# Kernel tuning notes

Hardware: AMD Instinct MI355X
Metric: run time of the kernel (lower is better)

## Reference

```python
import jax, jax.numpy as jnp
import numpy as np

HID = 256
NUM_LAYERS = 2


def setup_inputs() -> dict:
    key = jax.random.key(0)
    k0, k1, k2, k3 = jax.random.split(key, 4)
    B, R, C, I = 64, 32, 32, 8
    stdv = 1.0 / np.sqrt(HID)
    inp = jax.random.normal(k0, (B, R, C, I), jnp.float32)
    W_first = jax.random.uniform(k1, (6 * HID, I + 2 * HID), jnp.float32, -stdv, stdv)
    W_other = jax.random.uniform(k2, (NUM_LAYERS - 1, 6 * HID, 4 * HID), jnp.float32, -stdv, stdv)
    Bias = jax.random.uniform(k3, (NUM_LAYERS, 6 * HID), jnp.float32, -stdv, stdv)
    return {"input": inp, "W_first": W_first, "W_other": W_other, "Bias": Bias,
            "batch_size": B, "input_size": I, "flag": 0}


def _run_layer(a, W, b, H):
    # a: [R, B, L, F_in] diagonally-shifted input; W: [6H, F_in+2H]; b: [6H]
    R, Bb, L, _ = a.shape
    C = L - R + 1
    h0 = jnp.zeros((R, Bb, H), a.dtype)

    def step(carry, inputs):
        h_row, h_col = carry
        x_t, t = inputs
        z = jnp.concatenate([h_row, h_col, x_t], axis=-1)        # [R,B,2H+F]
        gate = jnp.einsum('rbf,gf->rbg', z, W)                   # [R,B,6H]
        # torch: bias added only to first B*(t+1) rows, and only when t < R
        mask = ((jnp.arange(R) <= t) & (t < R))[:, None, None]
        gate = jnp.where(mask, gate + b, gate)
        sig = jax.nn.sigmoid(gate[..., :4 * H])
        tnh = jnp.tanh(gate[..., 4 * H:])
        u_r, o_r, u_c, o_c = jnp.split(sig, 4, axis=-1)
        i_r, i_c = jnp.split(tnh, 2, axis=-1)
        h_row = jnp.tanh((1 - u_r) * h_row + u_r * i_r) * o_r
        h_col = jnp.tanh((1 - u_c) * h_col + u_c * i_c) * o_c
        out = jnp.concatenate([h_row, h_col], axis=-1)           # [R,B,2H]
        # row state that would be saved at this step (valid for t >= C-1)
        row_save = jax.lax.dynamic_index_in_dim(
            h_row, jnp.clip(t - (C - 1), 0, R - 1), axis=0, keepdims=False)
        col_save = h_col[R - 1]                                  # saved pre-roll
        h_col = jnp.roll(h_col, 1, axis=0)                       # roll by batch_size == shift slice axis by 1
        return (h_row, h_col), (out, row_save, col_save)

    xs = (jnp.moveaxis(a, 2, 0), jnp.arange(L))
    _, (outs, row_saves, col_saves) = jax.lax.scan(step, (h0, h0), xs)
    a_next = jnp.moveaxis(outs, 0, 2)        # [R, B, L, 2H]
    hidden_row = row_saves[C - 1:]           # [R, B, H]  (steps t >= C-1)
    hidden_col = col_saves[R - 1:]           # [C, B, H]  (steps t >= R-1)
    return a_next, hidden_row, hidden_col


def _forward(input, W_first, W_other, Bias, flag):
    H = Bias.shape[-1] // 6
    num_layers = Bias.shape[0]
    x = jnp.transpose(input, (2, 0, 1, 3)) if flag == 1 else jnp.transpose(input, (1, 0, 2, 3))
    R, Bb, C, I = x.shape
    L = R + C - 1
    # input_transfer[r, :, r:r+C, :] = x[r]  -> pad then roll each slice by r
    xp = jnp.pad(x, ((0, 0), (0, 0), (0, R - 1), (0, 0)))        # [R,B,L,I]
    a = jax.vmap(lambda xr, r: jnp.roll(xr, r, axis=1))(xp, jnp.arange(R))
    rows, cols = [], []
    for layer in range(num_layers):
        W = W_first if layer == 0 else W_other[layer - 1]
        a, hr, hc = _run_layer(a, W, Bias[layer], H)             # dropout=0 / eval: identity
        rows.append(hr)
        cols.append(hc)
    output_all = a.reshape(R * Bb, L, 2 * H)
    hidden_row_all = jnp.transpose(jnp.stack(rows), (2, 0, 1, 3))  # [B, NL, R, H]
    hidden_col_all = jnp.transpose(jnp.stack(cols), (2, 0, 1, 3))  # [B, NL, C, H]
    if flag == 1:
        return output_all, hidden_col_all, hidden_row_all
    return output_all, hidden_row_all, hidden_col_all


def reference(input, W_first, W_other, Bias, batch_size, input_size, flag):
    return _forward(input, W_first, W_other, Bias, flag)
```

## Files before the change

### kernel.cpp

```cpp
#include <hip/hip_runtime.h>

typedef __bf16 bf16x8 __attribute__((ext_vector_type(8)));
typedef float  f32x4  __attribute__((ext_vector_type(4)));

#define Z0S 520
#define Z1S 1032
#define W0P_ELEMS (2 * 8 * 17 * 6 * 512)
#define W1P_ELEMS (2 * 8 * 32 * 6 * 512)
#define XB_ELEMS (2 * 64 * 32 * 512)

__device__ __forceinline__ unsigned short f2bf(float f) {
    unsigned int u = __builtin_bit_cast(unsigned int, f);
    u += 0x7fffu + ((u >> 16) & 1u);
    return (unsigned short)(u >> 16);
}
__device__ __forceinline__ float sigm(float x) {
    x = fminf(30.f, fmaxf(-30.f, x));
    return __fdividef(1.0f, 1.0f + __expf(-x));
}
__device__ __forceinline__ float ftanh(float x) {
    x = fminf(15.f, fmaxf(-15.f, x));
    float e = __expf(2.0f * x);
    return 1.0f - __fdividef(2.0f, e + 1.0f);
}
__device__ __forceinline__ bf16x8 zero8() {
    bf16x8 v;
#pragma unroll
    for (int i = 0; i < 8; ++i) v[i] = (__bf16)0.0f;
    return v;
}
__device__ __forceinline__ void st_f32_wt(float* p, float v) {
    __hip_atomic_store(p, v, __ATOMIC_RELAXED, __HIP_MEMORY_SCOPE_AGENT);
}
__device__ __forceinline__ void st_u16_wt(unsigned short* p, unsigned short v) {
    __hip_atomic_store(p, v, __ATOMIC_RELAXED, __HIP_MEMORY_SCOPE_AGENT);
}

__global__ void convert_w(const float* __restrict__ W0f, const float* __restrict__ W1f,
                          unsigned short* __restrict__ W0p, unsigned short* __restrict__ W1p,
                          int* __restrict__ flags) {
    const int gid = blockIdx.x * blockDim.x + threadIdx.x;
    const int stride = gridDim.x * blockDim.x;
    if (gid < 512) flags[gid] = 0;
    for (int i = gid; i < W0P_ELEMS; i += stride) {
        const int e = i & 7, lane = (i >> 3) & 63;
        const int r = i >> 9;
        const int G = r % 6;  const int r2 = r / 6;
        const int ks = r2 % 17; const int gcg = r2 / 17;
        const int jj = gcg * 16 + (lane & 15);
        const int k = ks * 32 + (lane >> 4) * 8 + e;
        float v = 0.f;
        if (k < 520) v = W0f[(size_t)(G * 256 + jj) * 520 + k];
        W0p[i] = f2bf(v);
    }
    for (int i = gid; i < W1P_ELEMS; i += stride) {
        const int e = i & 7, lane = (i >> 3) & 63;
        const int r = i >> 9;
        const int G = r % 6;  const int r2 = r / 6;
        const int ks = r2 & 31; const int gcg = r2 >> 5;
        const int jj = gcg * 16 + (lane & 15);
        const int k = ks * 32 + (lane >> 4) * 8 + e;
        W1p[i] = f2bf(W1f[(size_t)(G * 256 + jj) * 1024 + k]);
    }
}

__global__ __launch_bounds__(512, 2) void witran_coop(
    const float* __restrict__ inp,
    const unsigned short* __restrict__ W0p,
    const unsigned short* __restrict__ W1p,
    const float* __restrict__ Bias,
    float* __restrict__ out,
    unsigned short* __restrict__ xb0,
    unsigned short* __restrict__ xb1,
    int* __restrict__ flags)
{
    const int bid  = blockIdx.x;
    const int r8   = bid & 7;
    const int s    = r8 >> 1;
    const int b    = (bid >> 3) * 2 + (r8 & 1);
    const int tid  = threadIdx.x;
    const int wave = tid >> 6;
    const int cg   = wave >> 1;
    const int mh   = wave & 1;
    const int lane = tid & 63;
    const int quad = lane >> 4;
    const int l16  = lane & 15;
    const int jl   = cg * 16 + l16;
    const int jj   = s * 64 + jl;
    const int gcg  = jj >> 4;

    int* f0 = flags;
    int* f1 = flags + 256;
    const int fown = b * 4 + s;

    __shared__ __align__(16) unsigned short z0[32 * Z0S];
    __shared__ __align__(16) unsigned short z1[32 * Z1S];
    __shared__ float rollbuf[32 * 64];

    for (int idx = tid; idx < 32 * Z0S; idx += 512) z0[idx] = 0;
    for (int idx = tid; idx < 32 * Z1S; idx += 512) z1[idx] = 0;
    __syncthreads();
    if (tid < 256) {
        const int m = tid >> 3, i = tid & 7;
        const int c = 0 - m;
        float v = 0.f;
        if (c >= 0 && c < 32) v = inp[((b * 32 + m) * 32 + c) * 8 + i];
        z0[m * Z0S + 512 + i] = f2bf(v);
    }

    float biasr[2][6];
#pragma unroll
    for (int L = 0; L < 2; ++L)
#pragma unroll
        for (int G = 0; G < 6; ++G)
            biasr[L][G] = Bias[L * 1536 + G * 256 + jj];

    float hrreg[2][4], hcreg[2][4], hcn[4];
#pragma unroll
    for (int L = 0; L < 2; ++L)
#pragma unroll
        for (int p = 0; p < 4; ++p) { hrreg[L][p] = 0.f; hcreg[L][p] = 0.f; }

    const unsigned short* w0w = W0p + (size_t)gcg * (17 * 6 * 512) + lane * 8;
    const unsigned short* w1w = W1p + (size_t)gcg * (32 * 6 * 512) + lane * 8;
    const unsigned short* aB0 = &z0[(mh * 16 + l16) * Z0S];
    const unsigned short* aB1 = &z1[(mh * 16 + l16) * Z1S];

    __syncthreads();

    const size_t OUT1 = 66060288u;
    const size_t OUT2 = OUT1 + 1048576u;

    const int sr   = tid >> 4;
    const int srem = tid & 15;
    const int sreg = srem >> 3;
    const int sc8  = (srem & 7) * 8;
    const int sr1  = (sr + 1) & 31;

    for (int t = 0; t < 63; ++t) {
        f32x4 acc[6];
        bf16x8 bA[6], bB[6];
#pragma unroll
        for (int G = 0; G < 6; ++G) acc[G] = (f32x4){0.f, 0.f, 0.f, 0.f};
#pragma unroll
        for (int G = 0; G < 6; ++G) bA[G] = *(const bf16x8*)&w0w[G * 512];

#pragma unroll 4
        for (int kp = 0; kp < 8; ++kp) {
            bf16x8 a0 = *(const bf16x8*)&aB0[(2 * kp) * 32 + quad * 8];
            bf16x8 a1 = *(const bf16x8*)&aB0[(2 * kp + 1) * 32 + quad * 8];
#pragma unroll
            for (int G = 0; G < 6; ++G) bB[G] = *(const bf16x8*)&w0w[((2 * kp + 1) * 6 + G) * 512];
#pragma unroll
            for (int G = 0; G < 6; ++G)
                acc[G] = __builtin_amdgcn_mfma_f32_16x16x32_bf16(a0, bA[G], acc[G], 0, 0, 0);
#pragma unroll
            for (int G = 0; G < 6; ++G) bA[G] = *(const bf16x8*)&w0w[((2 * kp + 2) * 6 + G) * 512];
#pragma unroll
            for (int G = 0; G < 6; ++G)
                acc[G] = __builtin_amdgcn_mfma_f32_16x16x32_bf16(a1, bB[G], acc[G], 0, 0, 0);
        }
        {
            bf16x8 a0 = zero8();
            if (quad == 0) a0 = *(const bf16x8*)&aB0[512];
#pragma unroll
            for (int G = 0; G < 6; ++G)
                acc[G] = __builtin_amdgcn_mfma_f32_16x16x32_bf16(a0, bA[G], acc[G], 0, 0, 0);
        }

#pragma unroll
        for (int p = 0; p < 4; ++p) {
            const int m = mh * 16 + quad * 4 + p;
            float g0 = acc[0][p], g1 = acc[1][p], g2 = acc[2][p];
            float g3 = acc[3][p], g4 = acc[4][p], g5 = acc[5][p];
            if ((t < 32) && (m <= t)) {
                g0 += biasr[0][0]; g1 += biasr[0][1]; g2 += biasr[0][2];
                g3 += biasr[0][3]; g4 += biasr[0][4]; g5 += biasr[0][5];
            }
            const float u_r = sigm(g0), o_r = sigm(g1), u_c = sigm(g2), o_c = sigm(g3);
            const float i_r = ftanh(g4), i_c = ftanh(g5);
            const float hrp = hrreg[0][p];
            const float hcp = hcreg[0][p];
            hrreg[0][p] = ftanh((1.f - u_r) * hrp + u_r * i_r) * o_r;
            hcn[p]      = ftanh((1.f - u_c) * hcp + u_c * i_c) * o_c;
        }
        __syncthreads();

#pragma unroll
        for (int p = 0; p < 4; ++p) {
            const int m  = mh * 16 + quad * 4 + p;
            const float hrf = hrreg[0][p];
            const float hcf = hcn[p];
            const unsigned short hrb = f2bf(hrf), hcb = f2bf(hcf);
            z0[m * Z0S + jj] = hrb;
            z0[((m + 1) & 31) * Z0S + 256 + jj] = hcb;
            z1[m * Z1S + 512 + jj] = hrb;
            z1[m * Z1S + 768 + jj] = hcb;
            rollbuf[m * 64 + jl] = hcf;
            const size_t xi = ((size_t)((t & 1) * 64 + b) * 32 + m) * 512;
            st_u16_wt(&xb0[xi + jj], hrb);
            st_u16_wt(&xb0[xi + 256 + jj], hcb);
            if (t >= 31) {
                if (m == t - 31) st_f32_wt(&out[OUT1 + ((size_t)(b * 2 + 0) * 32 + (t - 31)) * 256 + jj], hrf);
                if (m == 31)     st_f32_wt(&out[OUT2 + ((size_t)(b * 2 + 0) * 32 + (t - 31)) * 256 + jj], hcf);
            }
        }
        if (tid < 256 && t + 1 < 63) {
            const int m = tid >> 3, i = tid & 7;
            const int c = t + 1 - m;
            float v = 0.f;
            if (c >= 0 && c < 32) v = inp[((b * 32 + m) * 32 + c) * 8 + i];
            z0[m * Z0S + 512 + i] = f2bf(v);
        }
        __syncthreads();

        if (tid == 0)
            __hip_atomic_store(&f0[fown], t + 1, __ATOMIC_RELEASE, __HIP_MEMORY_SCOPE_AGENT);

#pragma unroll
        for (int p = 0; p < 4; ++p) {
            const int m = mh * 16 + quad * 4 + p;
            hcreg[0][p] = rollbuf[((m + 31) & 31) * 64 + jl];
        }

        if (tid == 0) {
#pragma unroll
            for (int j = 1; j < 4; ++j) {
                const int fp = b * 4 + ((s + j) & 3);
                int it = 0;
                while (__hip_atomic_load(&f0[fp], __ATOMIC_RELAXED, __HIP_MEMORY_SCOPE_AGENT) < t + 1) {
                    __builtin_amdgcn_s_sleep(4);
                    if (++it > 4000000) break;
                }
                it = 0;
                while (__hip_atomic_load(&f1[fp], __ATOMIC_RELAXED, __HIP_MEMORY_SCOPE_AGENT) < t) {
                    __builtin_amdgcn_s_sleep(4);
                    if (++it > 4000000) break;
                }
            }
        }
        __syncthreads();

        {
            const unsigned int* x0u = (const unsigned int*)xb0;
            const unsigned int* x1u = (const unsigned int*)xb1;
#pragma unroll
            for (int j = 1; j < 4; ++j) {
                const int q   = (s + j) & 3;
                const int col = q * 64 + sc8;
                union { unsigned int u4[4]; bf16x8 v; } q0, q1;
                const size_t e0 = (((size_t)((t & 1) * 64 + b) * 32 + sr) * 512 + sreg * 256 + col) >> 1;
#pragma unroll
                for (int w = 0; w < 4; ++w)
                    q0.u4[w] = __hip_atomic_load(&x0u[e0 + w], __ATOMIC_RELAXED, __HIP_MEMORY_SCOPE_AGENT);
                *(bf16x8*)&z1[sr * Z1S + 512 + sreg * 256 + col] = q0.v;
                *(bf16x8*)&z0[(sreg ? sr1 : sr) * Z0S + sreg * 256 + col] = q0.v;
                if (t > 0) {
                    const size_t e1 = (((size_t)(((t + 1) & 1) * 64 + b) * 32 + sr) * 512 + sreg * 256 + col) >> 1;
#pragma unroll
                    for (int w = 0; w < 4; ++w)
                        q1.u4[w] = __hip_atomic_load(&x1u[e1 + w], __ATOMIC_RELAXED, __HIP_MEMORY_SCOPE_AGENT);
                    *(bf16x8*)&z1[(sreg ? sr1 : sr) * Z1S + sreg * 256 + col] = q1.v;
                }
            }
        }
        __syncthreads();

#pragma unroll
        for (int G = 0; G < 6; ++G) acc[G] = (f32x4){0.f, 0.f, 0.f, 0.f};
#pragma unroll
        for (int G = 0; G < 6; ++G) bA[G] = *(const bf16x8*)&w1w[G * 512];

#pragma unroll 4
        for (int kp = 0; kp < 16; ++kp) {
            bf16x8 a0 = *(const bf16x8*)&aB1[(2 * kp) * 32 + quad * 8];
            bf16x8 a1 = *(const bf16x8*)&aB1[(2 * kp + 1) * 32 + quad * 8];
#pragma unroll
            for (int G = 0; G < 6; ++G) bB[G] = *(const bf16x8*)&w1w[((2 * kp + 1) * 6 + G) * 512];
#pragma unroll
            for (int G = 0; G < 6; ++G)
                acc[G] = __builtin_amdgcn_mfma_f32_16x16x32_bf16(a0, bA[G], acc[G], 0, 0, 0);
            const int kn = (kp < 15) ? (2 * kp + 2) : 31;
#pragma unroll
            for (int G = 0; G < 6; ++G) bA[G] = *(const bf16x8*)&w1w[(kn * 6 + G) * 512];
#pragma unroll
            for (int G = 0; G < 6; ++G)
                acc[G] = __builtin_amdgcn_mfma_f32_16x16x32_bf16(a1, bB[G], acc[G], 0, 0, 0);
        }

#pragma unroll
        for (int p = 0; p < 4; ++p) {
            const int m = mh * 16 + quad * 4 + p;
            float g0 = acc[0][p], g1 = acc[1][p], g2 = acc[2][p];
            float g3 = acc[3][p], g4 = acc[4][p], g5 = acc[5][p];
            if ((t < 32) && (m <= t)) {
                g0 += biasr[1][0]; g1 += biasr[1][1]; g2 += biasr[1][2];
                g3 += biasr[1][3]; g4 += biasr[1][4]; g5 += biasr[1][5];
            }
            const float u_r = sigm(g0), o_r = sigm(g1), u_c = sigm(g2), o_c = sigm(g3);
            const float i_r = ftanh(g4), i_c = ftanh(g5);
            const float hrp = hrreg[1][p];
            const float hcp = hcreg[1][p];
            hrreg[1][p] = ftanh((1.f - u_r) * hrp + u_r * i_r) * o_r;
            hcn[p]      = ftanh((1.f - u_c) * hcp + u_c * i_c) * o_c;
        }
        __syncthreads();

#pragma unroll
        for (int p = 0; p < 4; ++p) {
            const int m  = mh * 16 + quad * 4 + p;
            const float hrf = hrreg[1][p];
            const float hcf = hcn[p];
            const unsigned short hrb = f2bf(hrf), hcb = f2bf(hcf);
            z1[m * Z1S + jj] = hrb;
            z1[((m + 1) & 31) * Z1S + 256 + jj] = hcb;
            rollbuf[m * 64 + jl] = hcf;
            const size_t xi = ((size_t)((t & 1) * 64 + b) * 32 + m) * 512;
            st_u16_wt(&xb1[xi + jj], hrb);
            st_u16_wt(&xb1[xi + 256 + jj], hcb);
            const size_t row = (size_t)(m * 64 + b);
            st_f32_wt(&out[(row * 63 + t) * 512 + jj], hrf);
            st_f32_wt(&out[(row * 63 + t) * 512 + 256 + jj], hcf);
            if (t >= 31) {
                if (m == t - 31) st_f32_wt(&out[OUT1 + ((size_t)(b * 2 + 1) * 32 + (t - 31)) * 256 + jj], hrf);
                if (m == 31)     st_f32_wt(&out[OUT2 + ((size_t)(b * 2 + 1) * 32 + (t - 31)) * 256 + jj], hcf);
            }
        }
        __syncthreads();

        if (tid == 0)
            __hip_atomic_store(&f1[fown], t + 1, __ATOMIC_RELEASE, __HIP_MEMORY_SCOPE_AGENT);

#pragma unroll
        for (int p = 0; p < 4; ++p) {
            const int m = mh * 16 + quad * 4 + p;
            hcreg[1][p] = rollbuf[((m + 31) & 31) * 64 + jl];
        }
    }
}

extern "C" void kernel_launch(void* const* d_in, const int* in_sizes, int n_in,
                              void* d_out, int out_size, void* d_ws, size_t ws_size,
                              hipStream_t stream) {
    (void)in_sizes; (void)n_in; (void)out_size; (void)ws_size;
    const float* inp   = (const float*)d_in[0];
    const float* W0f   = (const float*)d_in[1];
    const float* W1f   = (const float*)d_in[2];
    const float* Biasf = (const float*)d_in[3];
    float* out = (float*)d_out;

    unsigned short* W0p = (unsigned short*)d_ws;
    unsigned short* W1p = W0p + W0P_ELEMS;
    int* flags = (int*)(W1p + W1P_ELEMS);
    unsigned short* xb0 = (unsigned short*)(flags + 512);
    unsigned short* xb1 = xb0 + XB_ELEMS;

    convert_w<<<dim3(512), dim3(256), 0, stream>>>(W0f, W1f, W0p, W1p, flags);
    witran_coop<<<dim3(256), dim3(512), 0, stream>>>(inp, W0p, W1p, Biasf, out,
                                                     xb0, xb1, flags);
}
```

Before: 2.211 ms.

## Split waves by gate group instead of row half to halve weight loads

Each wave pair now splits the six gates into a row-direction and a column-direction triple rather than splitting the 32 rows into two halves. Each wave computes both 16-row halves for its three gates. Every weight fragment loaded from global memory is therefore reused across two MFMAs, which halves per-wave weight traffic. The cost is more LDS A-fragment loads per wave, branch-divergent state write-back by gate group, and a different register footprint.

New measurement: 1.933 ms. 1.14x faster.

```diff
diff --git a/kernel.cpp b/kernel.cpp
--- a/kernel.cpp
+++ b/kernel.cpp
@@ -81,13 +81,14 @@
     const int tid  = threadIdx.x;
     const int wave = tid >> 6;
     const int cg   = wave >> 1;
-    const int mh   = wave & 1;
+    const int gh   = wave & 1;
     const int lane = tid & 63;
     const int quad = lane >> 4;
     const int l16  = lane & 15;
     const int jl   = cg * 16 + l16;
     const int jj   = s * 64 + jl;
     const int gcg  = jj >> 4;
+    const int Gs0 = 2 * gh, Gs1 = 2 * gh + 1, Gs2 = 4 + gh;
 
     int* f0 = flags;
     int* f1 = flags + 256;
@@ -108,23 +109,32 @@
         z0[m * Z0S + 512 + i] = f2bf(v);
     }
 
-    float biasr[2][6];
+    float biasr[2][3];
+#pragma unroll
+    for (int L = 0; L < 2; ++L) {
+        biasr[L][0] = Bias[L * 1536 + Gs0 * 256 + jj];
+        biasr[L][1] = Bias[L * 1536 + Gs1 * 256 + jj];
+        biasr[L][2] = Bias[L * 1536 + Gs2 * 256 + jj];
+    }
+
+    float streg[2][2][4];
 #pragma unroll
     for (int L = 0; L < 2; ++L)
 #pragma unroll
-        for (int G = 0; G < 6; ++G)
-            biasr[L][G] = Bias[L * 1536 + G * 256 + jj];
-
-    float hrreg[2][4], hcreg[2][4], hcn[4];
-#pragma unroll
-    for (int L = 0; L < 2; ++L)
-#pragma unroll
-        for (int p = 0; p < 4; ++p) { hrreg[L][p] = 0.f; hcreg[L][p] = 0.f; }
-
-    const unsigned short* w0w = W0p + (size_t)gcg * (17 * 6 * 512) + lane * 8;
-    const unsigned short* w1w = W1p + (size_t)gcg * (32 * 6 * 512) + lane * 8;
-    const unsigned short* aB0 = &z0[(mh * 16 + l16) * Z0S];
-    const unsigned short* aB1 = &z1[(mh * 16 + l16) * Z1S];
+        for (int mh = 0; mh < 2; ++mh)
+#pragma unroll
+            for (int p = 0; p < 4; ++p) streg[L][mh][p] = 0.f;
+
+    const unsigned short* w0g[3];
+    const unsigned short* w1g[3];
+    w0g[0] = W0p + (size_t)gcg * (17 * 6 * 512) + Gs0 * 512 + lane * 8;
+    w0g[1] = W0p + (size_t)gcg * (17 * 6 * 512) + Gs1 * 512 + lane * 8;
+    w0g[2] = W0p + (size_t)gcg * (17 * 6 * 512) + Gs2 * 512 + lane * 8;
+    w1g[0] = W1p + (size_t)gcg * (32 * 6 * 512) + Gs0 * 512 + lane * 8;
+    w1g[1] = W1p + (size_t)gcg * (32 * 6 * 512) + Gs1 * 512 + lane * 8;
+    w1g[2] = W1p + (size_t)gcg * (32 * 6 * 512) + Gs2 * 512 + lane * 8;
+    const unsigned short* aB0m[2] = { &z0[l16 * Z0S], &z0[(16 + l16) * Z0S] };
+    const unsigned short* aB1m[2] = { &z1[l16 * Z1S], &z1[(16 + l16) * Z1S] };
 
     __syncthreads();
 
@@ -138,73 +148,93 @@
     const int sr1  = (sr + 1) & 31;
 
     for (int t = 0; t < 63; ++t) {
-        f32x4 acc[6];
-        bf16x8 bA[6], bB[6];
-#pragma unroll
-        for (int G = 0; G < 6; ++G) acc[G] = (f32x4){0.f, 0.f, 0.f, 0.f};
-#pragma unroll
-        for (int G = 0; G < 6; ++G) bA[G] = *(const bf16x8*)&w0w[G * 512];
+        float snew[2][4];
+        f32x4 acc[3][2];
+        bf16x8 bA[3], bB[3];
+#pragma unroll
+        for (int i = 0; i < 3; ++i)
+#pragma unroll
+            for (int mh = 0; mh < 2; ++mh) acc[i][mh] = (f32x4){0.f, 0.f, 0.f, 0.f};
+#pragma unroll
+        for (int i = 0; i < 3; ++i) bA[i] = *(const bf16x8*)&w0g[i][0];
 
 #pragma unroll 4
         for (int kp = 0; kp < 8; ++kp) {
-            bf16x8 a0 = *(const bf16x8*)&aB0[(2 * kp) * 32 + quad * 8];
-            bf16x8 a1 = *(const bf16x8*)&aB0[(2 * kp + 1) * 32 + quad * 8];
-#pragma unroll
-            for (int G = 0; G < 6; ++G) bB[G] = *(const bf16x8*)&w0w[((2 * kp + 1) * 6 + G) * 512];
-#pragma unroll
-            for (int G = 0; G < 6; ++G)
-                acc[G] = __builtin_amdgcn_mfma_f32_16x16x32_bf16(a0, bA[G], acc[G], 0, 0, 0);
-#pragma unroll
-            for (int G = 0; G < 6; ++G) bA[G] = *(const bf16x8*)&w0w[((2 * kp + 2) * 6 + G) * 512];
-#pragma unroll
-            for (int G = 0; G < 6; ++G)
-                acc[G] = __builtin_amdgcn_mfma_f32_16x16x32_bf16(a1, bB[G], acc[G], 0, 0, 0);
+            bf16x8 a00 = *(const bf16x8*)&aB0m[0][(2 * kp) * 32 + quad * 8];
+            bf16x8 a01 = *(const bf16x8*)&aB0m[1][(2 * kp) * 32 + quad * 8];
+            bf16x8 a10 = *(const bf16x8*)&aB0m[0][(2 * kp + 1) * 32 + quad * 8];
+            bf16x8 a11 = *(const bf16x8*)&aB0m[1][(2 * kp + 1) * 32 + quad * 8];
+#pragma unroll
+            for (int i = 0; i < 3; ++i) bB[i] = *(const bf16x8*)&w0g[i][(2 * kp + 1) * 3072];
+#pragma unroll
+            for (int i = 0; i < 3; ++i) {
+                acc[i][0] = __builtin_amdgcn_mfma_f32_16x16x32_bf16(a00, bA[i], acc[i][0], 0, 0, 0);
+                acc[i][1] = __builtin_amdgcn_mfma_f32_16x16x32_bf16(a01, bA[i], acc[i][1], 0, 0, 0);
+            }
+#pragma unroll
+            for (int i = 0; i < 3; ++i) bA[i] = *(const bf16x8*)&w0g[i][(2 * kp + 2) * 3072];
+#pragma unroll
+            for (int i = 0; i < 3; ++i) {
+                acc[i][0] = __builtin_amdgcn_mfma_f32_16x16x32_bf16(a10, bB[i], acc[i][0], 0, 0, 0);
+                acc[i][1] = __builtin_amdgcn_mfma_f32_16x16x32_bf16(a11, bB[i], acc[i][1], 0, 0, 0);
+            }
         }
         {
-            bf16x8 a0 = zero8();
-            if (quad == 0) a0 = *(const bf16x8*)&aB0[512];
-#pragma unroll
-            for (int G = 0; G < 6; ++G)
-                acc[G] = __builtin_amdgcn_mfma_f32_16x16x32_bf16(a0, bA[G], acc[G], 0, 0, 0);
-        }
-
-#pragma unroll
-        for (int p = 0; p < 4; ++p) {
-            const int m = mh * 16 + quad * 4 + p;
-            float g0 = acc[0][p], g1 = acc[1][p], g2 = acc[2][p];
-            float g3 = acc[3][p], g4 = acc[4][p], g5 = acc[5][p];
-            if ((t < 32) && (m <= t)) {
-                g0 += biasr[0][0]; g1 += biasr[0][1]; g2 += biasr[0][2];
-                g3 += biasr[0][3]; g4 += biasr[0][4]; g5 += biasr[0][5];
-            }
-            const float u_r = sigm(g0), o_r = sigm(g1), u_c = sigm(g2), o_c = sigm(g3);
-            const float i_r = ftanh(g4), i_c = ftanh(g5);
-            const float hrp = hrreg[0][p];
-            const float hcp = hcreg[0][p];
-            hrreg[0][p] = ftanh((1.f - u_r) * hrp + u_r * i_r) * o_r;
-            hcn[p]      = ftanh((1.f - u_c) * hcp + u_c * i_c) * o_c;
-        }
-        __syncthreads();
-
-#pragma unroll
-        for (int p = 0; p < 4; ++p) {
-            const int m  = mh * 16 + quad * 4 + p;
-            const float hrf = hrreg[0][p];
-            const float hcf = hcn[p];
-            const unsigned short hrb = f2bf(hrf), hcb = f2bf(hcf);
-            z0[m * Z0S + jj] = hrb;
-            z0[((m + 1) & 31) * Z0S + 256 + jj] = hcb;
-            z1[m * Z1S + 512 + jj] = hrb;
-            z1[m * Z1S + 768 + jj] = hcb;
-            rollbuf[m * 64 + jl] = hcf;
-            const size_t xi = ((size_t)((t & 1) * 64 + b) * 32 + m) * 512;
-            st_u16_wt(&xb0[xi + jj], hrb);
-            st_u16_wt(&xb0[xi + 256 + jj], hcb);
-            if (t >= 31) {
-                if (m == t - 31) st_f32_wt(&out[OUT1 + ((size_t)(b * 2 + 0) * 32 + (t - 31)) * 256 + jj], hrf);
-                if (m == 31)     st_f32_wt(&out[OUT2 + ((size_t)(b * 2 + 0) * 32 + (t - 31)) * 256 + jj], hcf);
-            }
-        }
+            bf16x8 a0 = zero8(), a1 = zero8();
+            if (quad == 0) {
+                a0 = *(const bf16x8*)&aB0m[0][512];
+                a1 = *(const bf16x8*)&aB0m[1][512];
+            }
+#pragma unroll
+            for (int i = 0; i < 3; ++i) {
+                acc[i][0] = __builtin_amdgcn_mfma_f32_16x16x32_bf16(a0, bA[i], acc[i][0], 0, 0, 0);
+                acc[i][1] = __builtin_amdgcn_mfma_f32_16x16x32_bf16(a1, bA[i], acc[i][1], 0, 0, 0);
+            }
+        }
+
+#pragma unroll
+        for (int mh = 0; mh < 2; ++mh)
+#pragma unroll
+            for (int p = 0; p < 4; ++p) {
+                const int m = mh * 16 + quad * 4 + p;
+                float gu = acc[0][mh][p], go = acc[1][mh][p], gi = acc[2][mh][p];
+                if ((t < 32) && (m <= t)) {
+                    gu += biasr[0][0]; go += biasr[0][1]; gi += biasr[0][2];
+                }
+                const float u = sigm(gu), o = sigm(go), ii = ftanh(gi);
+                snew[mh][p] = ftanh((1.f - u) * streg[0][mh][p] + u * ii) * o;
+            }
+        if (gh == 0) {
+#pragma unroll
+            for (int mh = 0; mh < 2; ++mh)
+#pragma unroll
+                for (int p = 0; p < 4; ++p) streg[0][mh][p] = snew[mh][p];
+        }
+        __syncthreads();
+
+#pragma unroll
+        for (int mh = 0; mh < 2; ++mh)
+#pragma unroll
+            for (int p = 0; p < 4; ++p) {
+                const int m  = mh * 16 + quad * 4 + p;
+                const float f = snew[mh][p];
+                const unsigned short hb = f2bf(f);
+                const size_t xi = ((size_t)((t & 1) * 64 + b) * 32 + m) * 512;
+                if (gh == 0) {
+                    z0[m * Z0S + jj] = hb;
+                    z1[m * Z1S + 512 + jj] = hb;
+                    st_u16_wt(&xb0[xi + jj], hb);
+                    if (t >= 31 && m == t - 31)
+                        st_f32_wt(&out[OUT1 + ((size_t)(b * 2 + 0) * 32 + (t - 31)) * 256 + jj], f);
+                } else {
+                    z0[((m + 1) & 31) * Z0S + 256 + jj] = hb;
+                    z1[m * Z1S + 768 + jj] = hb;
+                    rollbuf[m * 64 + jl] = f;
+                    st_u16_wt(&xb0[xi + 256 + jj], hb);
+                    if (t >= 31 && m == 31)
+                        st_f32_wt(&out[OUT2 + ((size_t)(b * 2 + 0) * 32 + (t - 31)) * 256 + jj], f);
+                }
+            }
         if (tid < 256 && t + 1 < 63) {
             const int m = tid >> 3, i = tid & 7;
             const int c = t + 1 - m;
@@ -217,10 +247,14 @@
         if (tid == 0)
             __hip_atomic_store(&f0[fown], t + 1, __ATOMIC_RELEASE, __HIP_MEMORY_SCOPE_AGENT);
 
-#pragma unroll
-        for (int p = 0; p < 4; ++p) {
-            const int m = mh * 16 + quad * 4 + p;
-            hcreg[0][p] = rollbuf[((m + 31) & 31) * 64 + jl];
+        if (gh == 1) {
+#pragma unroll
+            for (int mh = 0; mh < 2; ++mh)
+#pragma unroll
+                for (int p = 0; p < 4; ++p) {
+                    const int m = mh * 16 + quad * 4 + p;
+                    streg[0][mh][p] = rollbuf[((m + 31) & 31) * 64 + jl];
+                }
         }
 
         if (tid == 0) {
@@ -267,74 +301,92 @@
         __syncthreads();
 
 #pragma unroll
-        for (int G = 0; G < 6; ++G) acc[G] = (f32x4){0.f, 0.f, 0.f, 0.f};
-#pragma unroll
-        for (int G = 0; G < 6; ++G) bA[G] = *(const bf16x8*)&w1w[G * 512];
+        for (int i = 0; i < 3; ++i)
+#pragma unroll
+            for (int mh = 0; mh < 2; ++mh) acc[i][mh] = (f32x4){0.f, 0.f, 0.f, 0.f};
+#pragma unroll
+        for (int i = 0; i < 3; ++i) bA[i] = *(const bf16x8*)&w1g[i][0];
 
 #pragma unroll 4
         for (int kp = 0; kp < 16; ++kp) {
-            bf16x8 a0 = *(const bf16x8*)&aB1[(2 * kp) * 32 + quad * 8];
-            bf16x8 a1 = *(const bf16x8*)&aB1[(2 * kp + 1) * 32 + quad * 8];
-#pragma unroll
-            for (int G = 0; G < 6; ++G) bB[G] = *(const bf16x8*)&w1w[((2 * kp + 1) * 6 + G) * 512];
-#pragma unroll
-            for (int G = 0; G < 6; ++G)
-                acc[G] = __builtin_amdgcn_mfma_f32_16x16x32_bf16(a0, bA[G], acc[G], 0, 0, 0);
+            bf16x8 a00 = *(const bf16x8*)&aB1m[0][(2 * kp) * 32 + quad * 8];
+            bf16x8 a01 = *(const bf16x8*)&aB1m[1][(2 * kp) * 32 + quad * 8];
+            bf16x8 a10 = *(const bf16x8*)&aB1m[0][(2 * kp + 1) * 32 + quad * 8];
+            bf16x8 a11 = *(const bf16x8*)&aB1m[1][(2 * kp + 1) * 32 + quad * 8];
+#pragma unroll
+            for (int i = 0; i < 3; ++i) bB[i] = *(const bf16x8*)&w1g[i][(2 * kp + 1) * 3072];
+#pragma unroll
+            for (int i = 0; i < 3; ++i) {
+                acc[i][0] = __builtin_amdgcn_mfma_f32_16x16x32_bf16(a00, bA[i], acc[i][0], 0, 0, 0);
+                acc[i][1] = __builtin_amdgcn_mfma_f32_16x16x32_bf16(a01, bA[i], acc[i][1], 0, 0, 0);
+            }
             const int kn = (kp < 15) ? (2 * kp + 2) : 31;
 #pragma unroll
-            for (int G = 0; G < 6; ++G) bA[G] = *(const bf16x8*)&w1w[(kn * 6 + G) * 512];
-#pragma unroll
-            for (int G = 0; G < 6; ++G)
-                acc[G] = __builtin_amdgcn_mfma_f32_16x16x32_bf16(a1, bB[G], acc[G], 0, 0, 0);
-        }
-
-#pragma unroll
-        for (int p = 0; p < 4; ++p) {
-            const int m = mh * 16 + quad * 4 + p;
-            float g0 = acc[0][p], g1 = acc[1][p], g2 = acc[2][p];
-            float g3 = acc[3][p], g4 = acc[4][p], g5 = acc[5][p];
-            if ((t < 32) && (m <= t)) {
-                g0 += biasr[1][0]; g1 += biasr[1][1]; g2 += biasr[1][2];
-                g3 += biasr[1][3]; g4 += biasr[1][4]; g5 += biasr[1][5];
-            }
-            const float u_r = sigm(g0), o_r = sigm(g1), u_c = sigm(g2), o_c = sigm(g3);
-            const float i_r = ftanh(g4), i_c = ftanh(g5);
-            const float hrp = hrreg[1][p];
-            const float hcp = hcreg[1][p];
-            hrreg[1][p] = ftanh((1.f - u_r) * hrp + u_r * i_r) * o_r;
-            hcn[p]      = ftanh((1.f - u_c) * hcp + u_c * i_c) * o_c;
-        }
-        __syncthreads();
-
-#pragma unroll
-        for (int p = 0; p < 4; ++p) {
-            const int m  = mh * 16 + quad * 4 + p;
-            const float hrf = hrreg[1][p];
-            const float hcf = hcn[p];
-            const unsigned short hrb = f2bf(hrf), hcb = f2bf(hcf);
-            z1[m * Z1S + jj] = hrb;
-            z1[((m + 1) & 31) * Z1S + 256 + jj] = hcb;
-            rollbuf[m * 64 + jl] = hcf;
-            const size_t xi = ((size_t)((t & 1) * 64 + b) * 32 + m) * 512;
-            st_u16_wt(&xb1[xi + jj], hrb);
-            st_u16_wt(&xb1[xi + 256 + jj], hcb);
-            const size_t row = (size_t)(m * 64 + b);
-            st_f32_wt(&out[(row * 63 + t) * 512 + jj], hrf);
-            st_f32_wt(&out[(row * 63 + t) * 512 + 256 + jj], hcf);
-            if (t >= 31) {
-                if (m == t - 31) st_f32_wt(&out[OUT1 + ((size_t)(b * 2 + 1) * 32 + (t - 31)) * 256 + jj], hrf);
-                if (m == 31)     st_f32_wt(&out[OUT2 + ((size_t)(b * 2 + 1) * 32 + (t - 31)) * 256 + jj], hcf);
-            }
-        }
+            for (int i = 0; i < 3; ++i) bA[i] = *(const bf16x8*)&w1g[i][kn * 3072];
+#pragma unroll
+            for (int i = 0; i < 3; ++i) {
+                acc[i][0] = __builtin_amdgcn_mfma_f32_16x16x32_bf16(a10, bB[i], acc[i][0], 0, 0, 0);
+                acc[i][1] = __builtin_amdgcn_mfma_f32_16x16x32_bf16(a11, bB[i], acc[i][1], 0, 0, 0);
+            }
+        }
+
+#pragma unroll
+        for (int mh = 0; mh < 2; ++mh)
+#pragma unroll
+            for (int p = 0; p < 4; ++p) {
+                const int m = mh * 16 + quad * 4 + p;
+                float gu = acc[0][mh][p], go = acc[1][mh][p], gi = acc[2][mh][p];
+                if ((t < 32) && (m <= t)) {
+                    gu += biasr[1][0]; go += biasr[1][1]; gi += biasr[1][2];
+                }
+                const float u = sigm(gu), o = sigm(go), ii = ftanh(gi);
+                snew[mh][p] = ftanh((1.f - u) * streg[1][mh][p] + u * ii) * o;
+            }
+        if (gh == 0) {
+#pragma unroll
+            for (int mh = 0; mh < 2; ++mh)
+#pragma unroll
+                for (int p = 0; p < 4; ++p) streg[1][mh][p] = snew[mh][p];
+        }
+        __syncthreads();
+
+#pragma unroll
+        for (int mh = 0; mh < 2; ++mh)
+#pragma unroll
+            for (int p = 0; p < 4; ++p) {
+                const int m  = mh * 16 + quad * 4 + p;
+                const float f = snew[mh][p];
+                const unsigned short hb = f2bf(f);
+                const size_t xi = ((size_t)((t & 1) * 64 + b) * 32 + m) * 512;
+                const size_t row = (size_t)(m * 64 + b);
+                if (gh == 0) {
+                    z1[m * Z1S + jj] = hb;
+                    st_u16_wt(&xb1[xi + jj], hb);
+                    st_f32_wt(&out[(row * 63 + t) * 512 + jj], f);
+                    if (t >= 31 && m == t - 31)
+                        st_f32_wt(&out[OUT1 + ((size_t)(b * 2 + 1) * 32 + (t - 31)) * 256 + jj], f);
+                } else {
+                    z1[((m + 1) & 31) * Z1S + 256 + jj] = hb;
+                    rollbuf[m * 64 + jl] = f;
+                    st_u16_wt(&xb1[xi + 256 + jj], hb);
+                    st_f32_wt(&out[(row * 63 + t) * 512 + 256 + jj], f);
+                    if (t >= 31 && m == 31)
+                        st_f32_wt(&out[OUT2 + ((size_t)(b * 2 + 1) * 32 + (t - 31)) * 256 + jj], f);
+                }
+            }
         __syncthreads();
 
         if (tid == 0)
             __hip_atomic_store(&f1[fown], t + 1, __ATOMIC_RELEASE, __HIP_MEMORY_SCOPE_AGENT);
 
-#pragma unroll
-        for (int p = 0; p < 4; ++p) {
-            const int m = mh * 16 + quad * 4 + p;
-            hcreg[1][p] = rollbuf[((m + 31) & 31) * 64 + jl];
+        if (gh == 1) {
+#pragma unroll
+            for (int mh = 0; mh < 2; ++mh)
+#pragma unroll
+                for (int p = 0; p < 4; ++p) {
+                    const int m = mh * 16 + quad * 4 + p;
+                    streg[1][mh][p] = rollbuf[((m + 31) & 31) * 64 + jl];
+                }
         }
     }
 }
```
